# Kernel optimization log

Hardware: AMD Instinct MI355X
Metric: run time of the kernel (lower is better)

## Reference

```python
import jax, jax.numpy as jnp
import numpy as np

N = 50000      # nodes
E = 500000     # edges (includes N self-loops)
DIN = 512
DOUT = 256
NEG_SLOPE = 0.01  # torch nn.LeakyReLU default


def setup_inputs() -> dict:
    key = jax.random.key(0)
    k1, k2, k3, k4, k5 = jax.random.split(key, 5)
    x = jax.random.normal(k1, (N, DIN), dtype=jnp.float32)
    # xavier_normal_ with gain=1.414
    std_W = 1.414 * np.sqrt(2.0 / (DIN + DOUT))
    W = jax.random.normal(k2, (DIN, DOUT), dtype=jnp.float32) * std_W
    std_a = 1.414 * np.sqrt(2.0 / (1 + 2 * DOUT))
    a = jax.random.normal(k3, (2 * DOUT,), dtype=jnp.float32) * std_a
    # first N edges are self-loops so every row-sum is nonzero
    loops = jnp.arange(N, dtype=jnp.int32)
    edge_src = jnp.concatenate([loops, jax.random.randint(k4, (E - N,), 0, N, dtype=jnp.int32)])
    edge_dst = jnp.concatenate([loops, jax.random.randint(k5, (E - N,), 0, N, dtype=jnp.int32)])
    return {"x": x, "W": W, "a": a, "edge_src": edge_src, "edge_dst": edge_dst}


def reference(x, W, a, edge_src, edge_dst):
    n = x.shape[0]
    d = W.shape[1]
    h = x @ W  # [N, DOUT]
    # a . [h_src ; h_dst] decomposed per-node, then gathered per-edge
    s_src = h @ a[:d]   # [N]
    s_dst = h @ a[d:]   # [N]
    score = s_src[edge_src] + s_dst[edge_dst]          # [E]
    e = jnp.exp(-jax.nn.leaky_relu(score, NEG_SLOPE))  # [E]
    # sparse softmax denominator: spmm(edge, e, ones) == segment sum over src
    e_rowsum = jax.ops.segment_sum(e, edge_src, num_segments=n)            # [N]
    # numerator: spmm(edge, e, h) == sum_j e_ij * h_j per row i
    h_prime = jax.ops.segment_sum(e[:, None] * h[edge_dst], edge_src, num_segments=n)  # [N, DOUT]
    h_prime = h_prime / e_rowsum[:, None]
    return jax.nn.elu(h_prime)  # concat=True branch
```

## Files before the change

kernel.cpp:

```cpp
#include <hip/hip_runtime.h>
#include <math.h>

#define DIN 512
#define DOUT 256
#define NEG_SLOPE 0.01f

typedef __attribute__((ext_vector_type(8))) short bf16x8;
typedef __attribute__((ext_vector_type(4))) float f32x4;
typedef __attribute__((ext_vector_type(4))) unsigned int u32x4;

__device__ __forceinline__ unsigned short f2bf(float f) {
    unsigned int u = __float_as_uint(f);
    unsigned int r = (u + 0x7FFFu + ((u >> 16) & 1u)) >> 16;
    return (unsigned short)r;
}
__device__ __forceinline__ float bf2f(unsigned short u) {
    return __uint_as_float(((unsigned int)u) << 16);
}
__device__ __forceinline__ unsigned int cvtpk(float lo, float hi) {
    unsigned int r;
    asm("v_cvt_pk_bf16_f32 %0, %1, %2" : "=v"(r) : "v"(lo), "v"(hi));
    return r;
}

__global__ void prep(const float* __restrict__ W, unsigned short* __restrict__ Bp,
                     int* __restrict__ deg, float* __restrict__ s_src,
                     float* __restrict__ s_dst, int N) {
    int t = blockIdx.x * blockDim.x + threadIdx.x;
    if (t < (DIN / 32) * (DOUT / 16) * 64) {
        int lane = t & 63;
        int cg = (t >> 6) & 15;
        int ks = t >> 10;
        int l15 = lane & 15, g = lane >> 4;
        int col = cg * 16 + l15;
        int k0 = ks * 32 + g * 8;
        ushort4 lo, hi;
        lo.x = f2bf(W[(size_t)(k0 + 0) * DOUT + col]);
        lo.y = f2bf(W[(size_t)(k0 + 1) * DOUT + col]);
        lo.z = f2bf(W[(size_t)(k0 + 2) * DOUT + col]);
        lo.w = f2bf(W[(size_t)(k0 + 3) * DOUT + col]);
        hi.x = f2bf(W[(size_t)(k0 + 4) * DOUT + col]);
        hi.y = f2bf(W[(size_t)(k0 + 5) * DOUT + col]);
        hi.z = f2bf(W[(size_t)(k0 + 6) * DOUT + col]);
        hi.w = f2bf(W[(size_t)(k0 + 7) * DOUT + col]);
        *(ushort4*)(Bp + (size_t)t * 8) = lo;
        *(ushort4*)(Bp + (size_t)t * 8 + 4) = hi;
    }
    if (t < N) { deg[t] = 0; s_src[t] = 0.f; s_dst[t] = 0.f; }
}

__global__ __launch_bounds__(64, 2) void gemm_k(const float* __restrict__ x,
                                                const unsigned short* __restrict__ Bp,
                                                unsigned short* __restrict__ hb,
                                                const float* __restrict__ av,
                                                float* __restrict__ s_src,
                                                float* __restrict__ s_dst, int M) {
    const int lane = threadIdx.x;
    const int l15 = lane & 15;
    const int g = lane >> 4;
    const int m0 = blockIdx.x * 32;
    const int half = blockIdx.y;

    int r0 = min(m0 + l15, M - 1);
    int r1 = min(m0 + 16 + l15, M - 1);
    const float* pA0 = x + (size_t)r0 * DIN + g * 8;
    const float* pA1 = x + (size_t)r1 * DIN + g * 8;
    const unsigned short* pB = Bp + ((size_t)(half * 8) * 64 + lane) * 8;

    f32x4 acc[2][8] = {};
    f32x4 abuf[2][4];
    bf16x8 bbuf[2][8];

#pragma unroll
    for (int i = 0; i < 2; ++i) {
        abuf[0][2 * i] = *(const f32x4*)((i ? pA1 : pA0));
        abuf[0][2 * i + 1] = *(const f32x4*)((i ? pA1 : pA0) + 4);
    }
#pragma unroll
    for (int cg = 0; cg < 8; ++cg)
        bbuf[0][cg] = *(const bf16x8*)(pB + (size_t)cg * 512);

#pragma unroll
    for (int ks = 0; ks < 16; ++ks) {
        const int cur = ks & 1;
        const int nxt = cur ^ 1;
        if (ks < 15) {
            const float* qA0 = pA0 + (ks + 1) * 32;
            const float* qA1 = pA1 + (ks + 1) * 32;
            abuf[nxt][0] = *(const f32x4*)qA0;
            abuf[nxt][1] = *(const f32x4*)(qA0 + 4);
            abuf[nxt][2] = *(const f32x4*)qA1;
            abuf[nxt][3] = *(const f32x4*)(qA1 + 4);
            const unsigned short* pBn = pB + (size_t)(ks + 1) * 16 * 512;
#pragma unroll
            for (int cg = 0; cg < 8; ++cg)
                bbuf[nxt][cg] = *(const bf16x8*)(pBn + (size_t)cg * 512);
        }
        u32x4 p;
        p.x = cvtpk(abuf[cur][0].x, abuf[cur][0].y);
        p.y = cvtpk(abuf[cur][0].z, abuf[cur][0].w);
        p.z = cvtpk(abuf[cur][1].x, abuf[cur][1].y);
        p.w = cvtpk(abuf[cur][1].z, abuf[cur][1].w);
        bf16x8 af0 = *(bf16x8*)&p;
        u32x4 q;
        q.x = cvtpk(abuf[cur][2].x, abuf[cur][2].y);
        q.y = cvtpk(abuf[cur][2].z, abuf[cur][2].w);
        q.z = cvtpk(abuf[cur][3].x, abuf[cur][3].y);
        q.w = cvtpk(abuf[cur][3].z, abuf[cur][3].w);
        bf16x8 af1 = *(bf16x8*)&q;
#pragma unroll
        for (int cg = 0; cg < 8; ++cg) {
            acc[0][cg] = __builtin_amdgcn_mfma_f32_16x16x32_bf16(af0, bbuf[cur][cg], acc[0][cg], 0, 0, 0);
            acc[1][cg] = __builtin_amdgcn_mfma_f32_16x16x32_bf16(af1, bbuf[cur][cg], acc[1][cg], 0, 0, 0);
        }
    }

    float as_[8], ad_[8];
#pragma unroll
    for (int cg = 0; cg < 8; ++cg) {
        int col = half * 128 + cg * 16 + l15;
        as_[cg] = av[col];
        ad_[cg] = av[DOUT + col];
    }
#pragma unroll
    for (int rf = 0; rf < 2; ++rf) {
#pragma unroll
        for (int j = 0; j < 4; ++j) {
            int row = m0 + rf * 16 + g * 4 + j;
            float ps = 0.f, pd = 0.f;
#pragma unroll
            for (int cg = 0; cg < 8; ++cg) {
                float v = acc[rf][cg][j];
                ps += v * as_[cg];
                pd += v * ad_[cg];
            }
#pragma unroll
            for (int off = 1; off < 16; off <<= 1) {
                ps += __shfl_xor(ps, off);
                pd += __shfl_xor(pd, off);
            }
            if (row < M) {
#pragma unroll
                for (int cg = 0; cg < 8; ++cg)
                    hb[(size_t)row * DOUT + half * 128 + cg * 16 + l15] = f2bf(acc[rf][cg][j]);
                if (l15 == 0) {
                    atomicAdd(&s_src[row], ps);
                    atomicAdd(&s_dst[row], pd);
                }
            }
        }
    }
}

__global__ void hist_k(const int* __restrict__ src, int* __restrict__ deg, int E) {
    int i = blockIdx.x * blockDim.x + threadIdx.x;
    if (i < E) atomicAdd(&deg[src[i]], 1);
}

__global__ __launch_bounds__(256) void block_sum(const int* __restrict__ deg, int* __restrict__ bsum, int N) {
    __shared__ int wsum[4];
    int b = blockIdx.x, t = threadIdx.x;
    int idx = b * 1024 + t * 4;
    int s = 0;
    if (idx + 3 < N) {
        int4 v = *(const int4*)(deg + idx);
        s = v.x + v.y + v.z + v.w;
    } else {
        for (int i = 0; i < 4; i++) if (idx + i < N) s += deg[idx + i];
    }
#pragma unroll
    for (int off = 32; off > 0; off >>= 1) s += __shfl_xor(s, off);
    if ((t & 63) == 0) wsum[t >> 6] = s;
    __syncthreads();
    if (t == 0) bsum[b] = wsum[0] + wsum[1] + wsum[2] + wsum[3];
}

__global__ void scan_tops(const int* __restrict__ bsum, int* __restrict__ boff,
                          int* __restrict__ rowptr, int nb, int N, int E) {
    int t = threadIdx.x;
    int v = (t < nb) ? bsum[t] : 0;
    int x = v;
#pragma unroll
    for (int off = 1; off < 64; off <<= 1) {
        int y = __shfl_up(x, off);
        if (t >= off) x += y;
    }
    if (t < nb) boff[t] = x - v;
    if (t == 0) rowptr[N] = E;
}

__global__ __launch_bounds__(256) void scan_blk(const int* __restrict__ deg, const int* __restrict__ boff,
                                                int* __restrict__ rowptr, int* __restrict__ cursor, int N) {
    __shared__ int wsum[4];
    int b = blockIdx.x, t = threadIdx.x;
    int idx = b * 1024 + t * 4;
    int v0 = 0, v1 = 0, v2 = 0, v3 = 0;
    if (idx + 3 < N) {
        int4 v = *(const int4*)(deg + idx);
        v0 = v.x; v1 = v.y; v2 = v.z; v3 = v.w;
    } else if (idx < N) {
        v0 = deg[idx];
        if (idx + 1 < N) v1 = deg[idx + 1];
        if (idx + 2 < N) v2 = deg[idx + 2];
    }
    int s = v0 + v1 + v2 + v3;
    int lane = t & 63, wid = t >> 6;
    int x = s;
#pragma unroll
    for (int off = 1; off < 64; off <<= 1) {
        int y = __shfl_up(x, off);
        if (lane >= off) x += y;
    }
    if (lane == 63) wsum[wid] = x;
    __syncthreads();
    int add = boff[b];
    for (int ww = 0; ww < wid; ++ww) add += wsum[ww];
    int e0 = add + x - s;
    int e1 = e0 + v0, e2 = e1 + v1, e3 = e2 + v2;
    if (idx < N)     { rowptr[idx] = e0;     cursor[idx] = e0; }
    if (idx + 1 < N) { rowptr[idx + 1] = e1; cursor[idx + 1] = e1; }
    if (idx + 2 < N) { rowptr[idx + 2] = e2; cursor[idx + 2] = e2; }
    if (idx + 3 < N) { rowptr[idx + 3] = e3; cursor[idx + 3] = e3; }
}

__global__ void edge_k(const int* __restrict__ src, const int* __restrict__ dst,
                       const float* __restrict__ s_src, const float* __restrict__ s_dst,
                       int* __restrict__ cursor, int2* __restrict__ csr, int E) {
    int i = blockIdx.x * blockDim.x + threadIdx.x;
    if (i >= E) return;
    int s = src[i], d = dst[i];
    float sc = s_src[s] + s_dst[d];
    float lrv = sc > 0.f ? sc : NEG_SLOPE * sc;
    float ev = __expf(-lrv);
    int pos = atomicAdd(&cursor[s], 1);
    csr[pos] = make_int2(d, __float_as_int(ev));
}

__global__ __launch_bounds__(256) void gather_k(const unsigned short* __restrict__ hb,
                                                const int* __restrict__ rowptr,
                                                const int2* __restrict__ csr,
                                                float* __restrict__ out, int N) {
    int gt = blockIdx.x * blockDim.x + threadIdx.x;
    int w = gt >> 6;
    int lane = threadIdx.x & 63;
    if (w >= N) return;
    int s0 = rowptr[w], s1 = rowptr[w + 1];
    float a0 = 0.f, a1 = 0.f, a2 = 0.f, a3 = 0.f, rs = 0.f;
    for (int base = s0; base < s1; base += 64) {
        int cnt = min(64, s1 - base);
        int dv = 0; float ev = 0.f;
        if (lane < cnt) {
            int2 p = csr[base + lane];
            dv = p.x; ev = __int_as_float(p.y);
        }
        int jj = 0;
        for (; jj + 4 <= cnt; jj += 4) {
            int d0 = __shfl(dv, jj), d1 = __shfl(dv, jj + 1), d2 = __shfl(dv, jj + 2), d3 = __shfl(dv, jj + 3);
            float e0 = __shfl(ev, jj), e1 = __shfl(ev, jj + 1), e2 = __shfl(ev, jj + 2), e3 = __shfl(ev, jj + 3);
            ushort4 h0 = *(const ushort4*)(hb + (size_t)d0 * DOUT + lane * 4);
            ushort4 h1 = *(const ushort4*)(hb + (size_t)d1 * DOUT + lane * 4);
            ushort4 h2 = *(const ushort4*)(hb + (size_t)d2 * DOUT + lane * 4);
            ushort4 h3 = *(const ushort4*)(hb + (size_t)d3 * DOUT + lane * 4);
            a0 += e0 * bf2f(h0.x) + e1 * bf2f(h1.x) + e2 * bf2f(h2.x) + e3 * bf2f(h3.x);
            a1 += e0 * bf2f(h0.y) + e1 * bf2f(h1.y) + e2 * bf2f(h2.y) + e3 * bf2f(h3.y);
            a2 += e0 * bf2f(h0.z) + e1 * bf2f(h1.z) + e2 * bf2f(h2.z) + e3 * bf2f(h3.z);
            a3 += e0 * bf2f(h0.w) + e1 * bf2f(h1.w) + e2 * bf2f(h2.w) + e3 * bf2f(h3.w);
            rs += e0 + e1 + e2 + e3;
        }
        for (; jj < cnt; ++jj) {
            int d0 = __shfl(dv, jj);
            float e0 = __shfl(ev, jj);
            ushort4 h0 = *(const ushort4*)(hb + (size_t)d0 * DOUT + lane * 4);
            a0 += e0 * bf2f(h0.x);
            a1 += e0 * bf2f(h0.y);
            a2 += e0 * bf2f(h0.z);
            a3 += e0 * bf2f(h0.w);
            rs += e0;
        }
    }
    float inv = 1.f / rs;
    float4 v;
    v.x = a0 * inv; v.y = a1 * inv; v.z = a2 * inv; v.w = a3 * inv;
    v.x = v.x > 0.f ? v.x : __expf(v.x) - 1.f;
    v.y = v.y > 0.f ? v.y : __expf(v.y) - 1.f;
    v.z = v.z > 0.f ? v.z : __expf(v.z) - 1.f;
    v.w = v.w > 0.f ? v.w : __expf(v.w) - 1.f;
    *(float4*)(out + (size_t)w * DOUT + lane * 4) = v;
}

extern "C" void kernel_launch(void* const* d_in, const int* in_sizes, int n_in,
                              void* d_out, int out_size, void* d_ws, size_t ws_size,
                              hipStream_t stream) {
    const float* x = (const float*)d_in[0];
    const float* W = (const float*)d_in[1];
    const float* a = (const float*)d_in[2];
    const int* edge_src = (const int*)d_in[3];
    const int* edge_dst = (const int*)d_in[4];

    const int N = in_sizes[0] / DIN;
    const int E = in_sizes[3];
    const int nb = (N + 1023) / 1024;

    char* ws = (char*)d_ws;
    size_t off = 0;
    auto alloc = [&](size_t bytes) {
        void* p = ws + off;
        off += (bytes + 15) & ~(size_t)15;
        return p;
    };
    unsigned short* hb = (unsigned short*)alloc((size_t)N * DOUT * 2);
    unsigned short* Bp = (unsigned short*)alloc((size_t)DIN * DOUT * 2);
    int* rowptr = (int*)alloc((size_t)(N + 1) * 4);
    int* deg = (int*)alloc((size_t)N * 4);
    int* cursor = (int*)alloc((size_t)N * 4);
    float* s_src = (float*)alloc((size_t)N * 4);
    float* s_dst = (float*)alloc((size_t)N * 4);
    int2* csr = (int2*)alloc((size_t)E * 8);
    int* bsum = (int*)alloc((size_t)nb * 4);
    int* boff = (int*)alloc((size_t)nb * 4);
    (void)ws_size;

    float* out = (float*)d_out;

    prep<<<(N + 255) / 256, 256, 0, stream>>>(W, Bp, deg, s_src, s_dst, N);
    hist_k<<<(E + 255) / 256, 256, 0, stream>>>(edge_src, deg, E);
    dim3 ggrid((N + 31) / 32, 2);
    gemm_k<<<ggrid, 64, 0, stream>>>(x, Bp, hb, a, s_src, s_dst, N);
    block_sum<<<nb, 256, 0, stream>>>(deg, bsum, N);
    scan_tops<<<1, 64, 0, stream>>>(bsum, boff, rowptr, nb, N, E);
    scan_blk<<<nb, 256, 0, stream>>>(deg, boff, rowptr, cursor, N);
    edge_k<<<(E + 255) / 256, 256, 0, stream>>>(edge_src, edge_dst, s_src, s_dst,
                                                cursor, csr, E);
    gather_k<<<(N + 3) / 4, 256, 0, stream>>>(hb, rowptr, csr, out, N);
}
```

Measured before the change: 174.9 us.

## Stage A tiles through LDS with async global_load_lds and swizzle

The x tile is now loaded with global_load_lds into a double-buffered, XOR-swizzled LDS buffer, and the per-step A fragments are read back from LDS. B fragments are loaded directly from global memory just before each MFMA instead of being register-prefetched. Occupancy is raised from 2 to 3 waves via launch bounds. The goal is coalesced loads of x and lower register pressure. The risks are that the waitcnt counting interacts with the B loads now issued inside the loop, B latency is no longer hidden, and there is no barrier even though each lane reads LDS data written by other lanes' loads.

```diff
diff --git a/kernel.cpp b/kernel.cpp
--- a/kernel.cpp
+++ b/kernel.cpp
@@ -21,6 +21,11 @@
     unsigned int r;
     asm("v_cvt_pk_bf16_f32 %0, %1, %2" : "=v"(r) : "v"(lo), "v"(hi));
     return r;
+}
+__device__ __forceinline__ void gload16(const void* g, void* l) {
+    __builtin_amdgcn_global_load_lds(
+        (const __attribute__((address_space(1))) void*)g,
+        (__attribute__((address_space(3))) void*)l, 16, 0, 0);
 }
 
 __global__ void prep(const float* __restrict__ W, unsigned short* __restrict__ Bp,
@@ -49,69 +54,65 @@
     if (t < N) { deg[t] = 0; s_src[t] = 0.f; s_dst[t] = 0.f; }
 }
 
-__global__ __launch_bounds__(64, 2) void gemm_k(const float* __restrict__ x,
+__global__ __launch_bounds__(64, 3) void gemm_k(const float* __restrict__ x,
                                                 const unsigned short* __restrict__ Bp,
                                                 unsigned short* __restrict__ hb,
                                                 const float* __restrict__ av,
                                                 float* __restrict__ s_src,
                                                 float* __restrict__ s_dst, int M) {
+    __shared__ unsigned char As[8192];
     const int lane = threadIdx.x;
     const int l15 = lane & 15;
     const int g = lane >> 4;
     const int m0 = blockIdx.x * 32;
     const int half = blockIdx.y;
 
-    int r0 = min(m0 + l15, M - 1);
-    int r1 = min(m0 + 16 + l15, M - 1);
-    const float* pA0 = x + (size_t)r0 * DIN + g * 8;
-    const float* pA1 = x + (size_t)r1 * DIN + g * 8;
+    auto stage = [&](int bb, int ks) {
+#pragma unroll
+        for (int it = 0; it < 4; ++it) {
+            int s = it * 64 + lane;
+            int row = s >> 3;
+            int slot = s & 7;
+            int q = slot ^ (row & 7);
+            int rg = min(m0 + row, M - 1);
+            const float* src = x + (size_t)rg * DIN + ks * 32 + q * 4;
+            gload16(src, As + bb * 4096 + it * 1024);
+        }
+    };
+
     const unsigned short* pB = Bp + ((size_t)(half * 8) * 64 + lane) * 8;
-
     f32x4 acc[2][8] = {};
-    f32x4 abuf[2][4];
-    bf16x8 bbuf[2][8];
-
-#pragma unroll
-    for (int i = 0; i < 2; ++i) {
-        abuf[0][2 * i] = *(const f32x4*)((i ? pA1 : pA0));
-        abuf[0][2 * i + 1] = *(const f32x4*)((i ? pA1 : pA0) + 4);
-    }
-#pragma unroll
-    for (int cg = 0; cg < 8; ++cg)
-        bbuf[0][cg] = *(const bf16x8*)(pB + (size_t)cg * 512);
-
+
+    stage(0, 0);
 #pragma unroll
     for (int ks = 0; ks < 16; ++ks) {
-        const int cur = ks & 1;
-        const int nxt = cur ^ 1;
+        const int bb = ks & 1;
         if (ks < 15) {
-            const float* qA0 = pA0 + (ks + 1) * 32;
-            const float* qA1 = pA1 + (ks + 1) * 32;
-            abuf[nxt][0] = *(const f32x4*)qA0;
-            abuf[nxt][1] = *(const f32x4*)(qA0 + 4);
-            abuf[nxt][2] = *(const f32x4*)qA1;
-            abuf[nxt][3] = *(const f32x4*)(qA1 + 4);
-            const unsigned short* pBn = pB + (size_t)(ks + 1) * 16 * 512;
-#pragma unroll
-            for (int cg = 0; cg < 8; ++cg)
-                bbuf[nxt][cg] = *(const bf16x8*)(pBn + (size_t)cg * 512);
-        }
+            stage(bb ^ 1, ks + 1);
+            asm volatile("s_waitcnt vmcnt(4)" ::: "memory");
+        } else {
+            asm volatile("s_waitcnt vmcnt(0)" ::: "memory");
+        }
+        const unsigned char* Ab = As + bb * 4096;
+        const int rr0 = l15, rr1 = l15 + 16;
+        f32x4 v0 = *(const f32x4*)(Ab + rr0 * 128 + (((2 * g) ^ (rr0 & 7)) << 4));
+        f32x4 v1 = *(const f32x4*)(Ab + rr0 * 128 + (((2 * g + 1) ^ (rr0 & 7)) << 4));
+        f32x4 w0 = *(const f32x4*)(Ab + rr1 * 128 + (((2 * g) ^ (rr1 & 7)) << 4));
+        f32x4 w1 = *(const f32x4*)(Ab + rr1 * 128 + (((2 * g + 1) ^ (rr1 & 7)) << 4));
         u32x4 p;
-        p.x = cvtpk(abuf[cur][0].x, abuf[cur][0].y);
-        p.y = cvtpk(abuf[cur][0].z, abuf[cur][0].w);
-        p.z = cvtpk(abuf[cur][1].x, abuf[cur][1].y);
-        p.w = cvtpk(abuf[cur][1].z, abuf[cur][1].w);
+        p.x = cvtpk(v0.x, v0.y); p.y = cvtpk(v0.z, v0.w);
+        p.z = cvtpk(v1.x, v1.y); p.w = cvtpk(v1.z, v1.w);
         bf16x8 af0 = *(bf16x8*)&p;
         u32x4 q;
-        q.x = cvtpk(abuf[cur][2].x, abuf[cur][2].y);
-        q.y = cvtpk(abuf[cur][2].z, abuf[cur][2].w);
-        q.z = cvtpk(abuf[cur][3].x, abuf[cur][3].y);
-        q.w = cvtpk(abuf[cur][3].z, abuf[cur][3].w);
+        q.x = cvtpk(w0.x, w0.y); q.y = cvtpk(w0.z, w0.w);
+        q.z = cvtpk(w1.x, w1.y); q.w = cvtpk(w1.z, w1.w);
         bf16x8 af1 = *(bf16x8*)&q;
+        const unsigned short* pBks = pB + (size_t)ks * 16 * 512;
 #pragma unroll
         for (int cg = 0; cg < 8; ++cg) {
-            acc[0][cg] = __builtin_amdgcn_mfma_f32_16x16x32_bf16(af0, bbuf[cur][cg], acc[0][cg], 0, 0, 0);
-            acc[1][cg] = __builtin_amdgcn_mfma_f32_16x16x32_bf16(af1, bbuf[cur][cg], acc[1][cg], 0, 0, 0);
+            bf16x8 bfr = *(const bf16x8*)(pBks + (size_t)cg * 512);
+            acc[0][cg] = __builtin_amdgcn_mfma_f32_16x16x32_bf16(af0, bfr, acc[0][cg], 0, 0, 0);
+            acc[1][cg] = __builtin_amdgcn_mfma_f32_16x16x32_bf16(af1, bfr, acc[1][cg], 0, 0, 0);
         }
     }
 
```

Result: faster. 147.3 us (-15.8%).
